# Kernel tuning notes

Hardware: AMD Instinct MI355X
Metric: run time of the kernel (lower is better)

## Reference

```python
import jax, jax.numpy as jnp
import numpy as np

MD = 4      # maxdisp
FAC = 1     # squeeze factor
WSIZE = 3   # truncation window half-size -> 7x7 maxpool over (u,v)

B, U, V, H, W = 64, 2 * MD + 1, 2 * (MD // FAC) + 1, 96, 96


def setup_inputs() -> dict:
    key = jax.random.key(0)
    x = jax.random.normal(key, (B, U, V, H, W), dtype=jnp.float32)
    return {"x": x}


def reference(x):
    b, u, v, h, w = x.shape
    # --- truncated winner-take-all mask ---
    flat = x.reshape(b, u * v, h, w)
    idx = jnp.argmax(flat, axis=1)                       # [b,h,w]
    mask = jax.nn.one_hot(idx, u * v, axis=1, dtype=x.dtype)  # [b,uv,h,w]
    mask = mask.reshape(b, u, v, h, w)
    # 3D maxpool with kernel (7,7,1) over (u,v), stride 1, pad 3 -> dilate winner
    k = 2 * WSIZE + 1
    mask = jax.lax.reduce_window(
        mask, -jnp.inf, jax.lax.max,
        window_dimensions=(1, k, k, 1, 1),
        window_strides=(1, 1, 1, 1, 1),
        padding=[(0, 0), (WSIZE, WSIZE), (WSIZE, WSIZE), (0, 0), (0, 0)],
    )
    xt = jnp.where(mask > 0, x, -jnp.inf)
    # --- softmax over displacement plane (truncated) ---
    p = jax.nn.softmax(xt.reshape(b, u * v, h, w), axis=1).reshape(b, u, v, h, w)
    # flowx varies along u (rows), flowy varies along v (cols) per torch meshgrid
    fx = jnp.arange(-MD, MD + 1, dtype=x.dtype).reshape(1, u, 1, 1, 1)
    fy = jnp.arange(-(MD // FAC), MD // FAC + 1, dtype=x.dtype).reshape(1, 1, v, 1, 1)
    outx = jnp.sum(p * fx, axis=(1, 2))[:, None]          # [b,1,h,w]
    outy = jnp.sum(p * fy, axis=(1, 2))[:, None]
    # --- local entropy (on truncated distribution) ---
    pc = jnp.clip(p, 1e-9, 1.0 - 1e-9)
    local_ent = (-(p * jnp.log(pc)).sum((1, 2)))[:, None] / np.log(float(k * k))
    # --- global entropy (on full distribution) ---
    pg = jax.nn.softmax(x.reshape(b, u * v, h, w), axis=1).reshape(b, u, v, h, w)
    pgc = jnp.clip(pg, 1e-9, 1.0 - 1e-9)
    global_ent = (-(pg * jnp.log(pgc)).sum((1, 2)))[:, None] / np.log(float(u * v))
    # flow (2ch) + entropy (2ch) concatenated -> [b,4,h,w]
    return jnp.concatenate([outx, outy, local_ent, global_ent], axis=1)
```

## Files before the change

### kernel.cpp

```cpp
#include <hip/hip_runtime.h>

#define NB 64
#define NU 9
#define NV 9
#define UV 81
#define HWSZ 9216
#define MDISP 4
#define WSZ 3

__global__ __launch_bounds__(256) void vcn_kernel(const float* __restrict__ x,
                                                  float* __restrict__ out) {
    int tid = blockIdx.x * blockDim.x + threadIdx.x;
    int b  = tid / HWSZ;
    int hw = tid - b * HWSZ;

    const float* xp = x + (size_t)b * UV * HWSZ + hw;

    float v[UV];
#pragma unroll
    for (int i = 0; i < UV; ++i) v[i] = xp[(size_t)i * HWSZ];

    float m = v[0];
    int idx = 0;
#pragma unroll
    for (int i = 1; i < UV; ++i) {
        if (v[i] > m) { m = v[i]; idx = i; }
    }

    int uc = idx / NV;
    int vc = idx - uc * NV;
    int ulo = uc - WSZ, uhi = uc + WSZ;
    int vlo = vc - WSZ, vhi = vc + WSZ;

    float se_g = 0.f;
    float sxg  = 0.f;
    float se_l = 0.f;
    float sxl  = 0.f;
    float sfx  = 0.f;
    float sfy  = 0.f;
#pragma unroll
    for (int u = 0; u < NU; ++u) {
#pragma unroll
        for (int w = 0; w < NV; ++w) {
            float t = v[u * NV + w] - m;
            float e = __expf(t);
            float et = e * t;
            se_g += e;
            sxg  += et;
            bool in = (u >= ulo) & (u <= uhi) & (w >= vlo) & (w <= vhi);
            if (in) {
                se_l += e;
                sxl  += et;
                sfx  += e * (float)(u - MDISP);
                sfy  += e * (float)(w - MDISP);
            }
        }
    }

    float inv_l = 1.f / se_l;
    float inv_g = 1.f / se_g;

    float outx = sfx * inv_l;
    float outy = sfy * inv_l;
    float lent = (__logf(se_l) - sxl * inv_l) * 0.25694895f;
    float gent = (__logf(se_g) - sxg * inv_g) * 0.22754075f;

    float* op = out + (size_t)b * 4 * HWSZ + hw;
    op[0 * HWSZ] = outx;
    op[1 * HWSZ] = outy;
    op[2 * HWSZ] = lent;
    op[3 * HWSZ] = gent;
}

extern "C" void kernel_launch(void* const* d_in, const int* in_sizes, int n_in,
                              void* d_out, int out_size, void* d_ws, size_t ws_size,
                              hipStream_t stream) {
    const float* x = (const float*)d_in[0];
    float* out = (float*)d_out;
    const int total = NB * HWSZ;
    const int block = 256;
    const int grid = total / block;
    vcn_kernel<<<grid, block, 0, stream>>>(x, out);
}
```

Before: 260.1 us.

## Process two pixels per thread with float2 loads and two-pass reload

Each thread now handles two adjacent pixels using 8-byte vector loads and stores. It no longer keeps all 81 values in registers: a first pass computes the argmax and a second pass reloads the inputs to build the softmax and entropy sums. The aim is to cut register pressure so occupancy rises, and to widen memory transactions. The cost is reading the input twice, which relies on the cache hierarchy to absorb the second read.

```diff
diff --git a/kernel.cpp b/kernel.cpp
--- a/kernel.cpp
+++ b/kernel.cpp
@@ -6,70 +6,87 @@
 #define UV 81
 #define HWSZ 9216
 #define MDISP 4
-#define WSZ 3
+
+typedef float f32x2 __attribute__((ext_vector_type(2)));
 
 __global__ __launch_bounds__(256) void vcn_kernel(const float* __restrict__ x,
                                                   float* __restrict__ out) {
     int tid = blockIdx.x * blockDim.x + threadIdx.x;
-    int b  = tid / HWSZ;
-    int hw = tid - b * HWSZ;
+    int pix = tid * 2;
+    int b   = pix / HWSZ;
+    int hw  = pix - b * HWSZ;
 
-    const float* xp = x + (size_t)b * UV * HWSZ + hw;
+    const f32x2* xp = (const f32x2*)(x + (size_t)b * UV * HWSZ + hw);
+    const int PSTR = HWSZ / 2;
 
-    float v[UV];
+    float m0 = -1e30f, m1 = -1e30f;
+    int   i0 = 0,      i1 = 0;
 #pragma unroll
-    for (int i = 0; i < UV; ++i) v[i] = xp[(size_t)i * HWSZ];
-
-    float m = v[0];
-    int idx = 0;
-#pragma unroll
-    for (int i = 1; i < UV; ++i) {
-        if (v[i] > m) { m = v[i]; idx = i; }
+    for (int i = 0; i < UV; ++i) {
+        f32x2 v = xp[(size_t)i * PSTR];
+        if (v.x > m0) { m0 = v.x; i0 = i; }
+        if (v.y > m1) { m1 = v.y; i1 = i; }
     }
 
-    int uc = idx / NV;
-    int vc = idx - uc * NV;
-    int ulo = uc - WSZ, uhi = uc + WSZ;
-    int vlo = vc - WSZ, vhi = vc + WSZ;
+    int uc0 = i0 / NV, vc0 = i0 - uc0 * NV;
+    int uc1 = i1 / NV, vc1 = i1 - uc1 * NV;
 
-    float se_g = 0.f;
-    float sxg  = 0.f;
-    float se_l = 0.f;
-    float sxl  = 0.f;
-    float sfx  = 0.f;
-    float sfy  = 0.f;
+    float seg0 = 0.f, sxg0 = 0.f, sel0 = 0.f, sxl0 = 0.f, sfx0 = 0.f, sfy0 = 0.f;
+    float seg1 = 0.f, sxg1 = 0.f, sel1 = 0.f, sxl1 = 0.f, sfx1 = 0.f, sfy1 = 0.f;
 #pragma unroll
     for (int u = 0; u < NU; ++u) {
+        bool ur0 = (u >= uc0 - 3) & (u <= uc0 + 3);
+        bool ur1 = (u >= uc1 - 3) & (u <= uc1 + 3);
+        float fu = (float)(u - MDISP);
 #pragma unroll
         for (int w = 0; w < NV; ++w) {
-            float t = v[u * NV + w] - m;
-            float e = __expf(t);
-            float et = e * t;
-            se_g += e;
-            sxg  += et;
-            bool in = (u >= ulo) & (u <= uhi) & (w >= vlo) & (w <= vhi);
-            if (in) {
-                se_l += e;
-                sxl  += et;
-                sfx  += e * (float)(u - MDISP);
-                sfy  += e * (float)(w - MDISP);
+            f32x2 v = xp[(size_t)(u * NV + w) * PSTR];
+            float fv = (float)(w - MDISP);
+
+            {
+                float t = v.x - m0;
+                float e = __expf(t);
+                seg0 += e;
+                sxg0 += e * t;
+                bool in = ur0 & (w >= vc0 - 3) & (w <= vc0 + 3);
+                float e0 = in ? e : 0.f;
+                sel0 += e0;
+                sxl0 += e0 * t;
+                sfx0 += e0 * fu;
+                sfy0 += e0 * fv;
+            }
+            {
+                float t = v.y - m1;
+                float e = __expf(t);
+                seg1 += e;
+                sxg1 += e * t;
+                bool in = ur1 & (w >= vc1 - 3) & (w <= vc1 + 3);
+                float e1 = in ? e : 0.f;
+                sel1 += e1;
+                sxl1 += e1 * t;
+                sfx1 += e1 * fu;
+                sfy1 += e1 * fv;
             }
         }
     }
 
-    float inv_l = 1.f / se_l;
-    float inv_g = 1.f / se_g;
+    const float KLOC = 0.25694895f;
+    const float KGLO = 0.22754075f;
 
-    float outx = sfx * inv_l;
-    float outy = sfy * inv_l;
-    float lent = (__logf(se_l) - sxl * inv_l) * 0.25694895f;
-    float gent = (__logf(se_g) - sxg * inv_g) * 0.22754075f;
+    float il0 = 1.f / sel0, ig0 = 1.f / seg0;
+    float il1 = 1.f / sel1, ig1 = 1.f / seg1;
 
-    float* op = out + (size_t)b * 4 * HWSZ + hw;
-    op[0 * HWSZ] = outx;
-    op[1 * HWSZ] = outy;
-    op[2 * HWSZ] = lent;
-    op[3 * HWSZ] = gent;
+    f32x2 outx, outy, lent, gent;
+    outx.x = sfx0 * il0;                       outx.y = sfx1 * il1;
+    outy.x = sfy0 * il0;                       outy.y = sfy1 * il1;
+    lent.x = (__logf(sel0) - sxl0 * il0) * KLOC; lent.y = (__logf(sel1) - sxl1 * il1) * KLOC;
+    gent.x = (__logf(seg0) - sxg0 * ig0) * KGLO; gent.y = (__logf(seg1) - sxg1 * ig1) * KGLO;
+
+    f32x2* op = (f32x2*)(out + (size_t)b * 4 * HWSZ + hw);
+    op[0 * PSTR] = outx;
+    op[1 * PSTR] = outy;
+    op[2 * PSTR] = lent;
+    op[3 * PSTR] = gent;
 }
 
 extern "C" void kernel_launch(void* const* d_in, const int* in_sizes, int n_in,
@@ -77,8 +94,8 @@
                               hipStream_t stream) {
     const float* x = (const float*)d_in[0];
     float* out = (float*)d_out;
-    const int total = NB * HWSZ;
+    const int total_threads = NB * HWSZ / 2;
     const int block = 256;
-    const int grid = total / block;
+    const int grid = total_threads / block;
     vcn_kernel<<<grid, block, 0, stream>>>(x, out);
 }
```

Measured after the change: 277.3 us. 1.07x slower.

## Split displacement reduction across waves with vectorized two-pass LDS reduction

Applied to the files above, without the earlier changes.

The kernel now splits the 81 displacement channels across the four waves of a block, and each lane handles four pixels with 128-bit loads. Partial sums, max and argmax are combined through shared memory. A second pass re-reads the input, expected to hit cache, to build the truncated local sums around the winning centre. The max subtraction before exp is dropped, which avoids holding all 81 values in registers but risks overflow for inputs with large magnitudes.

```diff
diff --git a/kernel.cpp b/kernel.cpp
--- a/kernel.cpp
+++ b/kernel.cpp
@@ -5,71 +5,130 @@
 #define NV 9
 #define UV 81
 #define HWSZ 9216
-#define MDISP 4
-#define WSZ 3
+#define BLK_PX 256
+#define NWAVE 4
 
-__global__ __launch_bounds__(256) void vcn_kernel(const float* __restrict__ x,
-                                                  float* __restrict__ out) {
-    int tid = blockIdx.x * blockDim.x + threadIdx.x;
-    int b  = tid / HWSZ;
-    int hw = tid - b * HWSZ;
+typedef float f32x4 __attribute__((ext_vector_type(4)));
 
-    const float* xp = x + (size_t)b * UV * HWSZ + hw;
+__global__ __launch_bounds__(256, 4) void vcn_fused(const float* __restrict__ x,
+                                                    float* __restrict__ out) {
+    __shared__ float red[NWAVE][4][BLK_PX];
+    __shared__ int   cent[BLK_PX];
 
-    float v[UV];
+    const int q    = threadIdx.x >> 6;
+    const int lane = threadIdx.x & 63;
+    const int blk  = blockIdx.x;
+    const int b    = blk / 36;
+    const int hw0  = (blk - b * 36) * BLK_PX;
+
+    const float* xb = x + (size_t)b * UV * HWSZ + hw0;
+    const int i0 = (q * UV) >> 2;
+    const int i1 = ((q + 1) * UV) >> 2;
+
+    float seg[4] = {0.f, 0.f, 0.f, 0.f};
+    float sxe[4] = {0.f, 0.f, 0.f, 0.f};
+    float mx[4]  = {-1e30f, -1e30f, -1e30f, -1e30f};
+    int   ix[4]  = {0, 0, 0, 0};
+
+    for (int i = i0; i < i1; ++i) {
+        f32x4 v = *(const f32x4*)(xb + (size_t)i * HWSZ + lane * 4);
 #pragma unroll
-    for (int i = 0; i < UV; ++i) v[i] = xp[(size_t)i * HWSZ];
-
-    float m = v[0];
-    int idx = 0;
-#pragma unroll
-    for (int i = 1; i < UV; ++i) {
-        if (v[i] > m) { m = v[i]; idx = i; }
-    }
-
-    int uc = idx / NV;
-    int vc = idx - uc * NV;
-    int ulo = uc - WSZ, uhi = uc + WSZ;
-    int vlo = vc - WSZ, vhi = vc + WSZ;
-
-    float se_g = 0.f;
-    float sxg  = 0.f;
-    float se_l = 0.f;
-    float sxl  = 0.f;
-    float sfx  = 0.f;
-    float sfy  = 0.f;
-#pragma unroll
-    for (int u = 0; u < NU; ++u) {
-#pragma unroll
-        for (int w = 0; w < NV; ++w) {
-            float t = v[u * NV + w] - m;
+        for (int j = 0; j < 4; ++j) {
+            float t = v[j];
             float e = __expf(t);
-            float et = e * t;
-            se_g += e;
-            sxg  += et;
-            bool in = (u >= ulo) & (u <= uhi) & (w >= vlo) & (w <= vhi);
-            if (in) {
-                se_l += e;
-                sxl  += et;
-                sfx  += e * (float)(u - MDISP);
-                sfy  += e * (float)(w - MDISP);
-            }
+            seg[j] += e;
+            sxe[j] = fmaf(t, e, sxe[j]);
+            if (t > mx[j]) { mx[j] = t; ix[j] = i; }
         }
     }
+#pragma unroll
+    for (int j = 0; j < 4; ++j) {
+        int p = lane * 4 + j;
+        red[q][0][p] = seg[j];
+        red[q][1][p] = sxe[j];
+        red[q][2][p] = mx[j];
+        red[q][3][p] = __int_as_float(ix[j]);
+    }
+    __syncthreads();
 
-    float inv_l = 1.f / se_l;
-    float inv_g = 1.f / se_g;
+    {
+        int p = q * 64 + lane;
+        float s = 0.f, sx = 0.f, m = -1e30f;
+        int id = 0;
+#pragma unroll
+        for (int qq = 0; qq < NWAVE; ++qq) {
+            s  += red[qq][0][p];
+            sx += red[qq][1][p];
+            float mm = red[qq][2][p];
+            int  ii  = __float_as_int(red[qq][3][p]);
+            if (mm > m) { m = mm; id = ii; }
+        }
+        float gent = (__logf(s) - sx / s) * 0.22754075f;
+        out[((size_t)b * 4 + 3) * HWSZ + hw0 + p] = gent;
+        int ucw = id / NV, vcw = id - ucw * NV;
+        cent[p] = ucw * 16 + vcw;
+    }
+    __syncthreads();
 
-    float outx = sfx * inv_l;
-    float outy = sfy * inv_l;
-    float lent = (__logf(se_l) - sxl * inv_l) * 0.25694895f;
-    float gent = (__logf(se_g) - sxg * inv_g) * 0.22754075f;
+    int uc[4], vc[4];
+#pragma unroll
+    for (int j = 0; j < 4; ++j) {
+        int c = cent[lane * 4 + j];
+        uc[j] = c >> 4;
+        vc[j] = c & 15;
+    }
+    float sel[4] = {0.f, 0.f, 0.f, 0.f};
+    float sxl[4] = {0.f, 0.f, 0.f, 0.f};
+    float sfx[4] = {0.f, 0.f, 0.f, 0.f};
+    float sfy[4] = {0.f, 0.f, 0.f, 0.f};
 
-    float* op = out + (size_t)b * 4 * HWSZ + hw;
-    op[0 * HWSZ] = outx;
-    op[1 * HWSZ] = outy;
-    op[2 * HWSZ] = lent;
-    op[3 * HWSZ] = gent;
+    int u = i0 / NV;
+    int v = i0 - u * NV;
+    for (int i = i0; i < i1; ++i) {
+        f32x4 vv = *(const f32x4*)(xb + (size_t)i * HWSZ + lane * 4);
+        float fu = (float)(u - 4);
+        float fv = (float)(v - 4);
+#pragma unroll
+        for (int j = 0; j < 4; ++j) {
+            float t = vv[j];
+            float e = __expf(t);
+            bool in = ((unsigned)(u - uc[j] + 3) <= 6u) &
+                      ((unsigned)(v - vc[j] + 3) <= 6u);
+            float e0 = in ? e : 0.f;
+            sel[j] += e0;
+            sxl[j] = fmaf(t,  e0, sxl[j]);
+            sfx[j] = fmaf(fu, e0, sfx[j]);
+            sfy[j] = fmaf(fv, e0, sfy[j]);
+        }
+        ++v;
+        if (v == NV) { v = 0; ++u; }
+    }
+#pragma unroll
+    for (int j = 0; j < 4; ++j) {
+        int p = lane * 4 + j;
+        red[q][0][p] = sel[j];
+        red[q][1][p] = sxl[j];
+        red[q][2][p] = sfx[j];
+        red[q][3][p] = sfy[j];
+    }
+    __syncthreads();
+
+    {
+        int p = q * 64 + lane;
+        float s = 0.f, sx = 0.f, fx = 0.f, fy = 0.f;
+#pragma unroll
+        for (int qq = 0; qq < NWAVE; ++qq) {
+            s  += red[qq][0][p];
+            sx += red[qq][1][p];
+            fx += red[qq][2][p];
+            fy += red[qq][3][p];
+        }
+        float inv = 1.f / s;
+        size_t obase = (size_t)b * 4 * HWSZ + hw0 + p;
+        out[obase]             = fx * inv;
+        out[obase + HWSZ]      = fy * inv;
+        out[obase + 2 * HWSZ]  = (__logf(s) - sx * inv) * 0.25694895f;
+    }
 }
 
 extern "C" void kernel_launch(void* const* d_in, const int* in_sizes, int n_in,
@@ -77,8 +136,6 @@
                               hipStream_t stream) {
     const float* x = (const float*)d_in[0];
     float* out = (float*)d_out;
-    const int total = NB * HWSZ;
-    const int block = 256;
-    const int grid = total / block;
-    vcn_kernel<<<grid, block, 0, stream>>>(x, out);
+    const int grid = NB * (HWSZ / BLK_PX);
+    vcn_fused<<<grid, 256, 0, stream>>>(x, out);
 }
```

After: 293.6 us. 12.9% more time.

## Stage input through LDS with 16-byte vector loads and one-wave blocks

Applied to the files above, without the earlier changes.

Each 64-thread block now loads its 64 pixels × 81 displacement planes into shared memory using float4 global loads, then each lane reads its 81 values from LDS. This replaces 81 scalar strided loads per thread with wider vectorized loads, and shrinks blocks to a single wave. The masked accumulation also becomes branch-free select plus fma. The cost is 21 KB of LDS per block, which limits occupancy, plus an extra LDS round trip and a barrier.

```diff
diff --git a/kernel.cpp b/kernel.cpp
--- a/kernel.cpp
+++ b/kernel.cpp
@@ -5,20 +5,36 @@
 #define NV 9
 #define UV 81
 #define HWSZ 9216
-#define MDISP 4
-#define WSZ 3
+#define TPX 64
 
-__global__ __launch_bounds__(256) void vcn_kernel(const float* __restrict__ x,
-                                                  float* __restrict__ out) {
-    int tid = blockIdx.x * blockDim.x + threadIdx.x;
-    int b  = tid / HWSZ;
-    int hw = tid - b * HWSZ;
+typedef float f32x4 __attribute__((ext_vector_type(4)));
 
-    const float* xp = x + (size_t)b * UV * HWSZ + hw;
+__global__ __launch_bounds__(64) void vcn_kernel(const float* __restrict__ x,
+                                                 float* __restrict__ out) {
+    __shared__ __align__(16) float lds[84 * TPX];
+
+    const int lane = threadIdx.x;
+    const int blk  = blockIdx.x;
+    const int b    = blk / 144;
+    const int hw0  = (blk - b * 144) * TPX;
+
+    const float* xb = x + (size_t)b * UV * HWSZ + hw0;
+
+    const int pj = lane >> 4;
+    const int px = (lane & 15) * 4;
+    f32x4* lds4 = (f32x4*)lds;
+#pragma unroll
+    for (int k = 0; k < 21; ++k) {
+        int p = 4 * k + pj;
+        p = p > 80 ? 80 : p;
+        f32x4 val = *(const f32x4*)(xb + (size_t)p * HWSZ + px);
+        lds4[k * 64 + lane] = val;
+    }
+    __syncthreads();
 
     float v[UV];
 #pragma unroll
-    for (int i = 0; i < UV; ++i) v[i] = xp[(size_t)i * HWSZ];
+    for (int i = 0; i < UV; ++i) v[i] = lds[i * TPX + lane];
 
     float m = v[0];
     int idx = 0;
@@ -26,50 +42,38 @@
     for (int i = 1; i < UV; ++i) {
         if (v[i] > m) { m = v[i]; idx = i; }
     }
-
     int uc = idx / NV;
     int vc = idx - uc * NV;
-    int ulo = uc - WSZ, uhi = uc + WSZ;
-    int vlo = vc - WSZ, vhi = vc + WSZ;
 
-    float se_g = 0.f;
-    float sxg  = 0.f;
-    float se_l = 0.f;
-    float sxl  = 0.f;
-    float sfx  = 0.f;
-    float sfy  = 0.f;
+    float seg = 0.f, sxg = 0.f, sel = 0.f, sxl = 0.f, sfx = 0.f, sfy = 0.f;
 #pragma unroll
     for (int u = 0; u < NU; ++u) {
+        bool ur = (u >= uc - 3) & (u <= uc + 3);
+        float fu = (float)(u - 4);
 #pragma unroll
         for (int w = 0; w < NV; ++w) {
             float t = v[u * NV + w] - m;
             float e = __expf(t);
-            float et = e * t;
-            se_g += e;
-            sxg  += et;
-            bool in = (u >= ulo) & (u <= uhi) & (w >= vlo) & (w <= vhi);
-            if (in) {
-                se_l += e;
-                sxl  += et;
-                sfx  += e * (float)(u - MDISP);
-                sfy  += e * (float)(w - MDISP);
-            }
+            seg += e;
+            sxg = fmaf(e, t, sxg);
+            bool in = ur & (w >= vc - 3) & (w <= vc + 3);
+            float e0 = in ? e : 0.f;
+            sel += e0;
+            sxl = fmaf(e0, t, sxl);
+            sfx = fmaf(e0, fu, sfx);
+            sfy = fmaf(e0, (float)(w - 4), sfy);
         }
     }
 
-    float inv_l = 1.f / se_l;
-    float inv_g = 1.f / se_g;
+    const float KLOC = 0.25694895f;
+    const float KGLO = 0.22754075f;
+    float il = 1.f / sel, ig = 1.f / seg;
 
-    float outx = sfx * inv_l;
-    float outy = sfy * inv_l;
-    float lent = (__logf(se_l) - sxl * inv_l) * 0.25694895f;
-    float gent = (__logf(se_g) - sxg * inv_g) * 0.22754075f;
-
-    float* op = out + (size_t)b * 4 * HWSZ + hw;
-    op[0 * HWSZ] = outx;
-    op[1 * HWSZ] = outy;
-    op[2 * HWSZ] = lent;
-    op[3 * HWSZ] = gent;
+    float* op = out + (size_t)b * 4 * HWSZ + hw0 + lane;
+    op[0 * HWSZ] = sfx * il;
+    op[1 * HWSZ] = sfy * il;
+    op[2 * HWSZ] = (__logf(sel) - sxl * il) * KLOC;
+    op[3 * HWSZ] = (__logf(seg) - sxg * ig) * KGLO;
 }
 
 extern "C" void kernel_launch(void* const* d_in, const int* in_sizes, int n_in,
@@ -77,8 +81,6 @@
                               hipStream_t stream) {
     const float* x = (const float*)d_in[0];
     float* out = (float*)d_out;
-    const int total = NB * HWSZ;
-    const int block = 256;
-    const int grid = total / block;
-    vcn_kernel<<<grid, block, 0, stream>>>(x, out);
+    const int grid = NB * (HWSZ / TPX);
+    vcn_kernel<<<grid, 64, 0, stream>>>(x, out);
 }
```

Result: no change. 260.0 us (-0.0%).
